# Kernel optimization log

Measured on AMD Instinct MI355X. Metric: run time of the kernel, lower is better.

## Reference

```python
import jax, jax.numpy as jnp
import numpy as np

TOP_K = 5

def setup_inputs() -> dict:
    key = jax.random.key(0)
    k1, k2, k3, k4 = jax.random.split(key, 4)
    B, L, N, D = 4, 1024, 16384, 256
    encoded = jax.random.normal(k1, (B, L, D), dtype=jnp.float32)
    memory = jax.random.normal(k2, (B, N, D), dtype=jnp.float32)
    W = jax.random.normal(k3, (D, D), dtype=jnp.float32) * (1.0 / np.sqrt(D))
    b = jax.random.normal(k4, (D,), dtype=jnp.float32) * 0.01
    return {"encoded": encoded, "memory": memory, "W": W, "b": b}

def _l2norm(x, eps=1e-12):
    # matches torch F.normalize(dim=-1): x / max(||x||, eps)
    n = jnp.sqrt(jnp.sum(x * x, axis=-1, keepdims=True))
    return x / jnp.maximum(n, eps)

def reference(encoded, memory, W, b):
    # encoded: [B,L,D], memory: [B,N,D]
    enc_n = _l2norm(encoded)
    mem_n = _l2norm(memory)
    # cosine similarity [B,L,N]
    sim = jnp.einsum('bld,bnd->bln', enc_n, mem_n)
    _, idx = jax.lax.top_k(sim, TOP_K)          # idx: [B,L,K]
    # per-batch gather of raw memory rows: [B,L,K,D]
    selected = jax.vmap(lambda m, i: m[i])(memory, idx)
    matched = jnp.mean(selected, axis=2)        # [B,L,D]
    out = (encoded + matched) @ W.T + b         # nn.Linear
    return out
```

## Files before the change

kernel.cpp:

```cpp
#include <hip/hip_runtime.h>
#include <math.h>
#include <float.h>

#define B_  4
#define L_  1024
#define N_  16384
#define D_  256
#define K_  5
#define NCH 16
#define CHUNK (N_/NCH)
#define RESC 16

typedef __attribute__((ext_vector_type(8))) short bf16x8;
typedef __attribute__((ext_vector_type(4))) float f32x4;

static __device__ __forceinline__ unsigned short f2bf(float f) {
    unsigned int u = __float_as_uint(f);
    unsigned int r = (u + 0x7FFFu + ((u >> 16) & 1u)) >> 16;
    return (unsigned short)r;
}

__global__ __launch_bounds__(256) void prep_kernel(
    const float* __restrict__ enc, const float* __restrict__ mem,
    float* __restrict__ invn, unsigned short* __restrict__ memn_bf,
    unsigned short* __restrict__ enc_bf)
{
    const int row = blockIdx.x * 4 + (threadIdx.x >> 6);
    const int lane = threadIdx.x & 63;
    if (row < B_ * N_) {
        float4 v = reinterpret_cast<const float4*>(mem + (size_t)row * D_)[lane];
        float ss = v.x*v.x + v.y*v.y + v.z*v.z + v.w*v.w;
        #pragma unroll
        for (int off = 32; off; off >>= 1) ss += __shfl_xor(ss, off, 64);
        float inv = 1.0f / fmaxf(sqrtf(ss), 1e-12f);
        if (lane == 0) invn[row] = inv;
        uint2 p;
        p.x = (unsigned)f2bf(v.x*inv) | ((unsigned)f2bf(v.y*inv) << 16);
        p.y = (unsigned)f2bf(v.z*inv) | ((unsigned)f2bf(v.w*inv) << 16);
        reinterpret_cast<uint2*>(memn_bf + (size_t)row * D_)[lane] = p;
    } else {
        int r2 = row - B_ * N_;
        if (r2 >= B_ * L_) return;
        float4 v = reinterpret_cast<const float4*>(enc + (size_t)r2 * D_)[lane];
        uint2 p;
        p.x = (unsigned)f2bf(v.x) | ((unsigned)f2bf(v.y) << 16);
        p.y = (unsigned)f2bf(v.z) | ((unsigned)f2bf(v.w) << 16);
        reinterpret_cast<uint2*>(enc_bf + (size_t)r2 * D_)[lane] = p;
    }
}

__global__ __launch_bounds__(256, 2) void screen_kernel(
    const unsigned short* __restrict__ enc_bf,
    const unsigned short* __restrict__ memn_bf,
    unsigned int* __restrict__ pcand)
{
    __shared__ __align__(16) union {
        struct { unsigned char A[128*128]; unsigned char Bt[128*128]; } st;
        unsigned int mg[128][41];
    } sm;

    const int tid = threadIdx.x;
    const int lane = tid & 63;
    const int wv = tid >> 6;
    const int wm = wv >> 1, wn = wv & 1;
    const int b = blockIdx.z;
    const int l0 = blockIdx.y * 128;
    const int ch = blockIdx.x;

    const int sq = tid & 7;
    const int sr0 = tid >> 3;

    const int ra = wm * 64 + (lane & 15);
    const int rb = wn * 64 + (lane & 15);
    const unsigned aswz = ((unsigned)(ra & 7)) << 4;
    const unsigned bswz = ((unsigned)(rb & 7)) << 4;
    const int kgB = (lane >> 4) * 16;
    const int g4 = (lane >> 4) * 4;

    const unsigned short* encB = enc_bf + ((size_t)b * L_ + l0) * D_;
    const unsigned short* memB = memn_bf + ((size_t)b * N_ + ch * CHUNK) * D_;

    unsigned tl[4][5];
    #pragma unroll
    for (int j = 0; j < 4; ++j)
        #pragma unroll
        for (int p = 0; p < 5; ++p) tl[j][p] = 0u;

    for (int nt = 0; nt < CHUNK / 128; ++nt) {
        const int n0 = nt * 128;
        f32x4 acc[4][4];
        #pragma unroll
        for (int i = 0; i < 4; ++i)
            #pragma unroll
            for (int j = 0; j < 4; ++j) acc[i][j] = (f32x4){0.f,0.f,0.f,0.f};

        for (int kt = 0; kt < D_ / 64; ++kt) {
            const int k0 = kt * 64;
            __syncthreads();
            #pragma unroll
            for (int i = 0; i < 4; ++i) {
                const int row = sr0 + i * 32;
                const int colw = (sq * 16) ^ ((row & 7) << 4);
                uint4 va = *reinterpret_cast<const uint4*>(
                    &memB[(size_t)(n0 + row) * D_ + k0 + sq * 8]);
                *reinterpret_cast<uint4*>(sm.st.A + row * 128 + colw) = va;
                uint4 vb = *reinterpret_cast<const uint4*>(
                    &encB[(size_t)row * D_ + k0 + sq * 8]);
                *reinterpret_cast<uint4*>(sm.st.Bt + row * 128 + colw) = vb;
            }
            __syncthreads();
            #pragma unroll
            for (int kk = 0; kk < 2; ++kk) {
                const int kb = kk * 64 + kgB;
                bf16x8 af[4], bfv[4];
                #pragma unroll
                for (int m = 0; m < 4; ++m)
                    af[m] = *reinterpret_cast<const bf16x8*>(
                        sm.st.A + (ra + m * 16) * 128 + (kb ^ aswz));
                #pragma unroll
                for (int n = 0; n < 4; ++n)
                    bfv[n] = *reinterpret_cast<const bf16x8*>(
                        sm.st.Bt + (rb + n * 16) * 128 + (kb ^ bswz));
                #pragma unroll
                for (int m = 0; m < 4; ++m)
                    #pragma unroll
                    for (int n = 0; n < 4; ++n)
                        acc[m][n] = __builtin_amdgcn_mfma_f32_16x16x32_bf16(
                            af[m], bfv[n], acc[m][n], 0, 0, 0);
            }
        }

        const unsigned inv_base = 1023u - (unsigned)(n0 + wm * 64 + g4);
        #pragma unroll
        for (int i = 0; i < 4; ++i) {
            #pragma unroll
            for (int r = 0; r < 4; ++r) {
                const unsigned idxv = inv_base - (unsigned)(i * 16 + r);
                #pragma unroll
                for (int j = 0; j < 4; ++j) {
                    float fb = acc[i][j][r] + 64.0f;
                    unsigned c = (__float_as_uint(fb) & 0xFFFFFC00u) | idxv;
                    #pragma unroll
                    for (int p = 0; p < 5; ++p) {
                        unsigned mx = tl[j][p] > c ? tl[j][p] : c;
                        unsigned mn = tl[j][p] > c ? c : tl[j][p];
                        tl[j][p] = mx; c = mn;
                    }
                }
            }
        }
    }

    __syncthreads();
    {
        const int c = lane & 15;
        const int src = wm * 4 + (lane >> 4);
        #pragma unroll
        for (int j = 0; j < 4; ++j) {
            const int l = wn * 64 + j * 16 + c;
            #pragma unroll
            for (int p = 0; p < 5; ++p)
                sm.mg[l][src * 5 + p] = tl[j][p];
        }
    }
    __syncthreads();

    if (tid < 128) {
        unsigned best[8];
        #pragma unroll
        for (int p = 0; p < 8; ++p) best[p] = 0u;
        #pragma unroll
        for (int c = 0; c < 40; ++c) {
            unsigned key = sm.mg[tid][c];
            #pragma unroll
            for (int p = 0; p < 8; ++p) {
                unsigned mx = best[p] > key ? best[p] : key;
                unsigned mn = best[p] > key ? key : best[p];
                best[p] = mx; key = mn;
            }
        }
        size_t gb = (((size_t)b * L_ + l0 + tid) * NCH + ch) * 8;
        #pragma unroll
        for (int p = 0; p < 8; ++p) pcand[gb + p] = best[p];
    }
}

__global__ __launch_bounds__(256) void rescore_kernel(
    const float* __restrict__ enc, const float* __restrict__ mem,
    const float* __restrict__ invn,
    const unsigned int* __restrict__ pcand,
    float* __restrict__ tbuf)
{
    __shared__ int cand_lds[4][RESC];
    const int wv = threadIdx.x >> 6;
    const int lane = threadIdx.x & 63;
    const int row = blockIdx.x * 4 + wv;
    const int b = row >> 10;
    const int l = row & 1023;

    const size_t cb = (size_t)row * (NCH * 8);
    unsigned k0 = pcand[cb + lane], k1 = pcand[cb + 64 + lane];

    #pragma unroll
    for (int rr = 0; rr < RESC; ++rr) {
        unsigned mv; int mi;
        bool t0 = (k0 >= k1);
        mv = t0 ? k0 : k1; mi = t0 ? lane : 64 + lane;
        #pragma unroll
        for (int off = 32; off; off >>= 1) {
            unsigned ov = __shfl_xor(mv, off, 64);
            int oi = __shfl_xor(mi, off, 64);
            if (ov > mv || (ov == mv && oi < mi)) { mv = ov; mi = oi; }
        }
        if (lane == 0) {
            int chunk = mi >> 3;
            cand_lds[wv][rr] = chunk * CHUNK + (CHUNK - 1) - (int)(mv & 0x3FFu);
        }
        if (mi == lane) k0 = 0u;
        if (mi == 64 + lane) k1 = 0u;
    }
    __syncthreads();

    const int ci = cand_lds[wv][lane >> 2];
    const int q = lane & 3;
    const float4* er = reinterpret_cast<const float4*>(enc + ((size_t)b * L_ + l) * D_) + q * 16;
    const float4* mr = reinterpret_cast<const float4*>(mem + ((size_t)b * N_ + ci) * D_) + q * 16;
    float s = 0.0f;
    #pragma unroll
    for (int k = 0; k < 16; ++k) {
        float4 e = er[k], m = mr[k];
        s = fmaf(e.x, m.x, s); s = fmaf(e.y, m.y, s);
        s = fmaf(e.z, m.z, s); s = fmaf(e.w, m.w, s);
    }
    s += __shfl_xor(s, 1, 64);
    s += __shfl_xor(s, 2, 64);
    s *= invn[b * N_ + ci];

    float sw = s;
    int m0, m1, m2, m3, m4;
    #define PICK(MK) { \
        float mv = sw; int mi = ci; \
        if (sw == -FLT_MAX) mi = 0x7fffffff; \
        _Pragma("unroll") \
        for (int off = 32; off; off >>= 1) { \
            float ov = __shfl_xor(mv, off, 64); \
            int oi = __shfl_xor(mi, off, 64); \
            if (ov > mv || (ov == mv && oi < mi)) { mv = ov; mi = oi; } \
        } \
        MK = mi; \
        if (ci == mi) sw = -FLT_MAX; \
    }
    PICK(m0); PICK(m1); PICK(m2); PICK(m3); PICK(m4);
    #undef PICK

    const float4* eb = reinterpret_cast<const float4*>(enc + ((size_t)b * L_ + l) * D_);
    const float4* mb = reinterpret_cast<const float4*>(mem + (size_t)b * N_ * D_);
    float4 e = eb[lane];
    float4 a0 = mb[(size_t)m0 * 64 + lane];
    float4 a1 = mb[(size_t)m1 * 64 + lane];
    float4 a2 = mb[(size_t)m2 * 64 + lane];
    float4 a3 = mb[(size_t)m3 * 64 + lane];
    float4 a4 = mb[(size_t)m4 * 64 + lane];
    float4 o;
    o.x = e.x + 0.2f * (a0.x + a1.x + a2.x + a3.x + a4.x);
    o.y = e.y + 0.2f * (a0.y + a1.y + a2.y + a3.y + a4.y);
    o.z = e.z + 0.2f * (a0.z + a1.z + a2.z + a3.z + a4.z);
    o.w = e.w + 0.2f * (a0.w + a1.w + a2.w + a3.w + a4.w);
    reinterpret_cast<float4*>(tbuf + (size_t)row * D_)[lane] = o;
}

__global__ __launch_bounds__(512) void linear_kernel(
    const float* __restrict__ tbuf, const float* __restrict__ W,
    const float* __restrict__ bias, float* __restrict__ out)
{
    __shared__ float t_s[16][D_];
    const int blk = blockIdx.x;
    const int b = blk >> 6;
    const int r0 = (blk & 63) << 4;
    const int tid = threadIdx.x;

    #pragma unroll
    for (int k = 0; k < 2; ++k) {
        int idx = k * 512 + tid;
        int row = idx >> 6, c4 = idx & 63;
        float4 v = reinterpret_cast<const float4*>(
            tbuf + ((size_t)b * L_ + r0 + row) * D_)[c4];
        *reinterpret_cast<float4*>(&t_s[row][c4 * 4]) = v;
    }
    __syncthreads();

    const int dout = tid & 255;
    const int half = tid >> 8;
    float accr[8];
    #pragma unroll
    for (int r = 0; r < 8; ++r) accr[r] = 0.0f;
    const float4* Wr = reinterpret_cast<const float4*>(W + (size_t)dout * D_);
    for (int d4 = 0; d4 < D_ / 4; ++d4) {
        float4 w = Wr[d4];
        #pragma unroll
        for (int r = 0; r < 8; ++r) {
            float4 t = *reinterpret_cast<const float4*>(&t_s[half * 8 + r][d4 * 4]);
            accr[r] = fmaf(w.x, t.x, accr[r]);
            accr[r] = fmaf(w.y, t.y, accr[r]);
            accr[r] = fmaf(w.z, t.z, accr[r]);
            accr[r] = fmaf(w.w, t.w, accr[r]);
        }
    }
    float bb = bias[dout];
    #pragma unroll
    for (int r = 0; r < 8; ++r)
        out[((size_t)b * L_ + r0 + half * 8 + r) * D_ + dout] = accr[r] + bb;
}

extern "C" void kernel_launch(void* const* d_in, const int* in_sizes, int n_in,
                              void* d_out, int out_size, void* d_ws, size_t ws_size,
                              hipStream_t stream)
{
    (void)in_sizes; (void)n_in; (void)out_size;
    const float* enc  = (const float*)d_in[0];
    const float* mem  = (const float*)d_in[1];
    const float* W    = (const float*)d_in[2];
    const float* bias = (const float*)d_in[3];
    float* out = (float*)d_out;

    const size_t sz_memn = (size_t)B_ * N_ * D_ * 2;
    const size_t sz_enc  = (size_t)B_ * L_ * D_ * 2;
    const size_t sz_invn = (size_t)B_ * N_ * 4;
    const size_t sz_pc   = (size_t)B_ * L_ * NCH * 8 * 4;
    const size_t sz_tbuf = (size_t)B_ * L_ * D_ * 4;
    const size_t need = sz_memn + sz_enc + sz_invn + sz_pc + sz_tbuf;
    if (ws_size < need) return;

    char* p = (char*)d_ws;
    unsigned short* memn_bf = (unsigned short*)p;  p += sz_memn;
    unsigned short* enc_bf  = (unsigned short*)p;  p += sz_enc;
    float* invn = (float*)p;  p += sz_invn;
    unsigned int* pcand = (unsigned int*)p;  p += sz_pc;
    float* tbuf = (float*)p;

    {
        int rows = B_ * N_ + B_ * L_;
        prep_kernel<<<(rows + 3) / 4, 256, 0, stream>>>(enc, mem, invn, memn_bf, enc_bf);
    }
    {
        dim3 grid(NCH, L_ / 128, B_);
        screen_kernel<<<grid, 256, 0, stream>>>(enc_bf, memn_bf, pcand);
    }
    {
        rescore_kernel<<<(B_ * L_) / 4, 256, 0, stream>>>(enc, mem, invn, pcand, tbuf);
    }
    {
        linear_kernel<<<B_ * L_ / 16, 512, 0, stream>>>(tbuf, W, bias, out);
    }
}
```

Baseline: 206.7 us.

## Pipeline screen tiles with resident encoder LDS and fuse rescore with linear

The screen kernel now keeps the whole 128-row encoder tile resident in LDS, loaded once with global_load_lds. Memory tiles are streamed through direct-to-LDS loads, and accumulators are double-buffered so the top-5 fold of the previous tile interleaves with the MFMAs of the current tile. The score bias changes from +64 to a clamp at zero. The rescore and linear kernels are merged into one tail kernel that selects candidates with a ballot-based radix threshold instead of 16 serial argmax reductions, which removes the tbuf round trip and one launch. Risks are the 80KB LDS per block, which may reduce occupancy below two blocks per CU, and the clamp, which drops ordering among negative similarities.

```diff
diff --git a/kernel.cpp b/kernel.cpp
--- a/kernel.cpp
+++ b/kernel.cpp
@@ -18,6 +18,12 @@
     unsigned int u = __float_as_uint(f);
     unsigned int r = (u + 0x7FFFu + ((u >> 16) & 1u)) >> 16;
     return (unsigned short)r;
+}
+
+static __device__ __forceinline__ void gld16(const void* g, void* l) {
+    __builtin_amdgcn_global_load_lds(
+        (const __attribute__((address_space(1))) unsigned int*)g,
+        (__attribute__((address_space(3))) unsigned int*)l, 16, 0, 0);
 }
 
 __global__ __launch_bounds__(256) void prep_kernel(
@@ -49,15 +55,72 @@
     }
 }
 
+#define SCREEN_TILE(N0, ACC, PACC, PN0, DOFOLD)                                        \
+  {                                                                                    \
+    _Pragma("unroll")                                                                  \
+    for (int i_ = 0; i_ < 4; ++i_)                                                     \
+      _Pragma("unroll")                                                                \
+      for (int j_ = 0; j_ < 4; ++j_) ACC[i_][j_] = (f32x4){0.f, 0.f, 0.f, 0.f};        \
+    const char* memT_ = memBb + (size_t)(N0) * (D_ * 2);                               \
+    _Pragma("unroll")                                                                  \
+    for (int kt = 0; kt < 4; ++kt) {                                                   \
+      __syncthreads();                                                                 \
+      _Pragma("unroll")                                                                \
+      for (int c_ = 0; c_ < 4; ++c_) {                                                 \
+        int s_ = c_ * 4 + wv;                                                          \
+        gld16(memT_ + (size_t)(s_ * 8 + (lane >> 3)) * (D_ * 2) + kt * 128 + scolA,    \
+              sA + s_ * 1024);                                                         \
+      }                                                                                \
+      __syncthreads();                                                                 \
+      _Pragma("unroll")                                                                \
+      for (int kk = 0; kk < 2; ++kk) {                                                 \
+        const int kbA_ = kk * 64 + kgB;                                                \
+        const int cB_ = kt * 128 + kk * 64 + kgB;                                      \
+        bf16x8 af_[4], bfv_[4];                                                        \
+        _Pragma("unroll")                                                              \
+        for (int m_ = 0; m_ < 4; ++m_)                                                 \
+          af_[m_] = *reinterpret_cast<const bf16x8*>(                                  \
+              sA + (ra + m_ * 16) * 128 + (kbA_ ^ aswz));                              \
+        _Pragma("unroll")                                                              \
+        for (int n_ = 0; n_ < 4; ++n_)                                                 \
+          bfv_[n_] = *reinterpret_cast<const bf16x8*>(                                 \
+              sEnc + (rb + n_ * 16) * 512 + (cB_ ^ bswz));                             \
+        _Pragma("unroll")                                                              \
+        for (int m_ = 0; m_ < 4; ++m_)                                                 \
+          _Pragma("unroll")                                                            \
+          for (int n_ = 0; n_ < 4; ++n_)                                               \
+            ACC[m_][n_] = __builtin_amdgcn_mfma_f32_16x16x32_bf16(                     \
+                af_[m_], bfv_[n_], ACC[m_][n_], 0, 0, 0);                              \
+      }                                                                                \
+      if (DOFOLD) {                                                                    \
+        const unsigned ibase_ = 1023u - (unsigned)((PN0) + wm * 64 + kt * 16 + g4);    \
+        _Pragma("unroll")                                                              \
+        for (int r_ = 0; r_ < 4; ++r_) {                                               \
+          const unsigned idxv_ = ibase_ - (unsigned)r_;                                \
+          _Pragma("unroll")                                                            \
+          for (int j_ = 0; j_ < 4; ++j_) {                                             \
+            unsigned c2_ = (__float_as_uint(fmaxf(PACC[kt][j_][r_], 0.0f))             \
+                            & 0xFFFFFC00u) | idxv_;                                    \
+            _Pragma("unroll")                                                          \
+            for (int p_ = 0; p_ < 5; ++p_) {                                           \
+              unsigned mx_ = tl[j_][p_] > c2_ ? tl[j_][p_] : c2_;                      \
+              unsigned mn_ = tl[j_][p_] > c2_ ? c2_ : tl[j_][p_];                      \
+              tl[j_][p_] = mx_; c2_ = mn_;                                             \
+            }                                                                          \
+          }                                                                            \
+        }                                                                              \
+      }                                                                                \
+    }                                                                                  \
+  }
+
 __global__ __launch_bounds__(256, 2) void screen_kernel(
     const unsigned short* __restrict__ enc_bf,
     const unsigned short* __restrict__ memn_bf,
     unsigned int* __restrict__ pcand)
 {
-    __shared__ __align__(16) union {
-        struct { unsigned char A[128*128]; unsigned char Bt[128*128]; } st;
-        unsigned int mg[128][41];
-    } sm;
+    __shared__ __align__(16) unsigned char smem[16*1024 + 64*1024];
+    unsigned char* sA = smem;
+    unsigned char* sEnc = smem + 16*1024;
 
     const int tid = threadIdx.x;
     const int lane = tid & 63;
@@ -67,18 +130,24 @@
     const int l0 = blockIdx.y * 128;
     const int ch = blockIdx.x;
 
-    const int sq = tid & 7;
-    const int sr0 = tid >> 3;
-
     const int ra = wm * 64 + (lane & 15);
     const int rb = wn * 64 + (lane & 15);
     const unsigned aswz = ((unsigned)(ra & 7)) << 4;
     const unsigned bswz = ((unsigned)(rb & 7)) << 4;
     const int kgB = (lane >> 4) * 16;
     const int g4 = (lane >> 4) * 4;
-
-    const unsigned short* encB = enc_bf + ((size_t)b * L_ + l0) * D_;
-    const unsigned short* memB = memn_bf + ((size_t)b * N_ + ch * CHUNK) * D_;
+    const int scolA = ((lane & 7) * 16) ^ ((lane >> 3) << 4);
+
+    const char* encBb = (const char*)(enc_bf + ((size_t)b * L_ + l0) * D_);
+    const char* memBb = (const char*)(memn_bf + ((size_t)b * N_ + ch * CHUNK) * D_);
+
+    #pragma unroll
+    for (int c = 0; c < 16; ++c) {
+        int s = c * 4 + wv;
+        int row = s * 2 + (lane >> 5);
+        int col = ((lane & 31) * 16) ^ ((row & 7) << 4);
+        gld16(encBb + (size_t)row * 512 + col, sEnc + s * 1024);
+    }
 
     unsigned tl[4][5];
     #pragma unroll
@@ -86,65 +155,36 @@
         #pragma unroll
         for (int p = 0; p < 5; ++p) tl[j][p] = 0u;
 
-    for (int nt = 0; nt < CHUNK / 128; ++nt) {
-        const int n0 = nt * 128;
-        f32x4 acc[4][4];
-        #pragma unroll
-        for (int i = 0; i < 4; ++i)
-            #pragma unroll
-            for (int j = 0; j < 4; ++j) acc[i][j] = (f32x4){0.f,0.f,0.f,0.f};
-
-        for (int kt = 0; kt < D_ / 64; ++kt) {
-            const int k0 = kt * 64;
-            __syncthreads();
-            #pragma unroll
-            for (int i = 0; i < 4; ++i) {
-                const int row = sr0 + i * 32;
-                const int colw = (sq * 16) ^ ((row & 7) << 4);
-                uint4 va = *reinterpret_cast<const uint4*>(
-                    &memB[(size_t)(n0 + row) * D_ + k0 + sq * 8]);
-                *reinterpret_cast<uint4*>(sm.st.A + row * 128 + colw) = va;
-                uint4 vb = *reinterpret_cast<const uint4*>(
-                    &encB[(size_t)row * D_ + k0 + sq * 8]);
-                *reinterpret_cast<uint4*>(sm.st.Bt + row * 128 + colw) = vb;
-            }
-            __syncthreads();
-            #pragma unroll
-            for (int kk = 0; kk < 2; ++kk) {
-                const int kb = kk * 64 + kgB;
-                bf16x8 af[4], bfv[4];
-                #pragma unroll
-                for (int m = 0; m < 4; ++m)
-                    af[m] = *reinterpret_cast<const bf16x8*>(
-                        sm.st.A + (ra + m * 16) * 128 + (kb ^ aswz));
-                #pragma unroll
-                for (int n = 0; n < 4; ++n)
-                    bfv[n] = *reinterpret_cast<const bf16x8*>(
-                        sm.st.Bt + (rb + n * 16) * 128 + (kb ^ bswz));
-                #pragma unroll
-                for (int m = 0; m < 4; ++m)
-                    #pragma unroll
-                    for (int n = 0; n < 4; ++n)
-                        acc[m][n] = __builtin_amdgcn_mfma_f32_16x16x32_bf16(
-                            af[m], bfv[n], acc[m][n], 0, 0, 0);
-            }
-        }
-
-        const unsigned inv_base = 1023u - (unsigned)(n0 + wm * 64 + g4);
+    f32x4 accA[4][4], accB[4][4];
+
+    SCREEN_TILE(0, accA, accB, 0, false)
+    {
+        int n0v = 128, pn0v = 0;
+        #pragma unroll 1
+        for (int it = 0; it < 3; ++it) {
+            SCREEN_TILE(n0v, accB, accA, pn0v, true)
+            SCREEN_TILE(n0v + 128, accA, accB, pn0v + 128, true)
+            n0v += 256; pn0v += 256;
+        }
+    }
+    SCREEN_TILE(896, accB, accA, 768, true)
+
+    {
         #pragma unroll
         for (int i = 0; i < 4; ++i) {
+            const unsigned ibase = 1023u - (unsigned)(896 + wm * 64 + i * 16 + g4);
             #pragma unroll
             for (int r = 0; r < 4; ++r) {
-                const unsigned idxv = inv_base - (unsigned)(i * 16 + r);
+                const unsigned idxv = ibase - (unsigned)r;
                 #pragma unroll
                 for (int j = 0; j < 4; ++j) {
-                    float fb = acc[i][j][r] + 64.0f;
-                    unsigned c = (__float_as_uint(fb) & 0xFFFFFC00u) | idxv;
+                    unsigned c2 = (__float_as_uint(fmaxf(accB[i][j][r], 0.0f))
+                                   & 0xFFFFFC00u) | idxv;
                     #pragma unroll
                     for (int p = 0; p < 5; ++p) {
-                        unsigned mx = tl[j][p] > c ? tl[j][p] : c;
-                        unsigned mn = tl[j][p] > c ? c : tl[j][p];
-                        tl[j][p] = mx; c = mn;
+                        unsigned mx = tl[j][p] > c2 ? tl[j][p] : c2;
+                        unsigned mn = tl[j][p] > c2 ? c2 : tl[j][p];
+                        tl[j][p] = mx; c2 = mn;
                     }
                 }
             }
@@ -152,6 +192,7 @@
     }
 
     __syncthreads();
+    unsigned (*mg)[41] = reinterpret_cast<unsigned (*)[41]>(smem);
     {
         const int c = lane & 15;
         const int src = wm * 4 + (lane >> 4);
@@ -160,7 +201,7 @@
             const int l = wn * 64 + j * 16 + c;
             #pragma unroll
             for (int p = 0; p < 5; ++p)
-                sm.mg[l][src * 5 + p] = tl[j][p];
+                mg[l][src * 5 + p] = tl[j][p];
         }
     }
     __syncthreads();
@@ -171,7 +212,7 @@
         for (int p = 0; p < 8; ++p) best[p] = 0u;
         #pragma unroll
         for (int c = 0; c < 40; ++c) {
-            unsigned key = sm.mg[tid][c];
+            unsigned key = mg[tid][c];
             #pragma unroll
             for (int p = 0; p < 8; ++p) {
                 unsigned mx = best[p] > key ? best[p] : key;
@@ -185,112 +226,102 @@
     }
 }
 
-__global__ __launch_bounds__(256) void rescore_kernel(
+__global__ __launch_bounds__(256) void tail_kernel(
     const float* __restrict__ enc, const float* __restrict__ mem,
     const float* __restrict__ invn,
     const unsigned int* __restrict__ pcand,
-    float* __restrict__ tbuf)
+    const float* __restrict__ W, const float* __restrict__ bias,
+    float* __restrict__ out)
 {
-    __shared__ int cand_lds[4][RESC];
+    __shared__ float t_s[8][D_];
+    __shared__ int cand_s[4][RESC];
     const int wv = threadIdx.x >> 6;
     const int lane = threadIdx.x & 63;
-    const int row = blockIdx.x * 4 + wv;
-    const int b = row >> 10;
-    const int l = row & 1023;
-
-    const size_t cb = (size_t)row * (NCH * 8);
-    unsigned k0 = pcand[cb + lane], k1 = pcand[cb + 64 + lane];
-
-    #pragma unroll
-    for (int rr = 0; rr < RESC; ++rr) {
-        unsigned mv; int mi;
-        bool t0 = (k0 >= k1);
-        mv = t0 ? k0 : k1; mi = t0 ? lane : 64 + lane;
-        #pragma unroll
-        for (int off = 32; off; off >>= 1) {
-            unsigned ov = __shfl_xor(mv, off, 64);
-            int oi = __shfl_xor(mi, off, 64);
-            if (ov > mv || (ov == mv && oi < mi)) { mv = ov; mi = oi; }
-        }
-        if (lane == 0) {
-            int chunk = mi >> 3;
-            cand_lds[wv][rr] = chunk * CHUNK + (CHUNK - 1) - (int)(mv & 0x3FFu);
-        }
-        if (mi == lane) k0 = 0u;
-        if (mi == 64 + lane) k1 = 0u;
+    const int row0 = blockIdx.x * 8 + wv * 2;
+
+    #pragma unroll 1
+    for (int r2 = 0; r2 < 2; ++r2) {
+        const int row = row0 + r2;
+        const int b = row >> 10;
+        const int l = row & 1023;
+
+        const size_t cb = (size_t)row * (NCH * 8);
+        unsigned k0 = pcand[cb + lane], k1 = pcand[cb + 64 + lane];
+
+        unsigned v = 0;
+        #pragma unroll
+        for (int bit = 31; bit >= 0; --bit) {
+            unsigned t = v | (1u << bit);
+            int c = __popcll(__ballot(k0 >= t)) + __popcll(__ballot(k1 >= t));
+            v = (c >= RESC) ? t : v;
+        }
+        unsigned long long bA0 = __ballot(k0 > v), bA1 = __ballot(k1 > v);
+        unsigned long long bE0 = __ballot(k0 == v), bE1 = __ballot(k1 == v);
+        const int nA0 = __popcll(bA0);
+        const int nA = nA0 + __popcll(bA1);
+        const int need = RESC - nA;
+        const unsigned long long lt = (1ull << lane) - 1ull;
+        int s0 = -1, s1 = -1;
+        if (k0 > v) s0 = __popcll(bA0 & lt);
+        else if (k0 == v) { int r = __popcll(bE0 & lt); if (r < need) s0 = nA + r; }
+        if (k1 > v) s1 = nA0 + __popcll(bA1 & lt);
+        else if (k1 == v) { int r = __popcll(bE0) + __popcll(bE1 & lt); if (r < need) s1 = nA + r; }
+        if (s0 >= 0)
+            cand_s[wv][s0] = (lane >> 3) * CHUNK + (CHUNK - 1) - (int)(k0 & 1023u);
+        if (s1 >= 0)
+            cand_s[wv][s1] = (8 + (lane >> 3)) * CHUNK + (CHUNK - 1) - (int)(k1 & 1023u);
+        asm volatile("s_waitcnt lgkmcnt(0)" ::: "memory");
+
+        const int ci = cand_s[wv][lane >> 2];
+        const int q = lane & 3;
+        const float4* er = reinterpret_cast<const float4*>(enc + ((size_t)b * L_ + l) * D_) + q * 16;
+        const float4* mr = reinterpret_cast<const float4*>(mem + ((size_t)b * N_ + ci) * D_) + q * 16;
+        float s = 0.0f;
+        #pragma unroll
+        for (int k = 0; k < 16; ++k) {
+            float4 e = er[k], m = mr[k];
+            s = fmaf(e.x, m.x, s); s = fmaf(e.y, m.y, s);
+            s = fmaf(e.z, m.z, s); s = fmaf(e.w, m.w, s);
+        }
+        s += __shfl_xor(s, 1, 64);
+        s += __shfl_xor(s, 2, 64);
+        s *= invn[b * N_ + ci];
+
+        float sw = s;
+        int m0, m1, m2, m3, m4;
+        #define PICK(MK) { \
+            float mv = sw; int mi = ci; \
+            if (sw == -FLT_MAX) mi = 0x7fffffff; \
+            _Pragma("unroll") \
+            for (int off = 32; off >= 4; off >>= 1) { \
+                float ov = __shfl_xor(mv, off, 64); \
+                int oi = __shfl_xor(mi, off, 64); \
+                if (ov > mv || (ov == mv && oi < mi)) { mv = ov; mi = oi; } \
+            } \
+            MK = mi; \
+            if (ci == mi) sw = -FLT_MAX; \
+        }
+        PICK(m0); PICK(m1); PICK(m2); PICK(m3); PICK(m4);
+        #undef PICK
+
+        const float4* eb = reinterpret_cast<const float4*>(enc + ((size_t)b * L_ + l) * D_);
+        const float4* mb = reinterpret_cast<const float4*>(mem + (size_t)b * N_ * D_);
+        float4 e = eb[lane];
+        float4 a0 = mb[(size_t)m0 * 64 + lane];
+        float4 a1 = mb[(size_t)m1 * 64 + lane];
+        float4 a2 = mb[(size_t)m2 * 64 + lane];
+        float4 a3 = mb[(size_t)m3 * 64 + lane];
+        float4 a4 = mb[(size_t)m4 * 64 + lane];
+        float4 o;
+        o.x = e.x + 0.2f * (a0.x + a1.x + a2.x + a3.x + a4.x);
+        o.y = e.y + 0.2f * (a0.y + a1.y + a2.y + a3.y + a4.y);
+        o.z = e.z + 0.2f * (a0.z + a1.z + a2.z + a3.z + a4.z);
+        o.w = e.w + 0.2f * (a0.w + a1.w + a2.w + a3.w + a4.w);
+        *reinterpret_cast<float4*>(&t_s[wv * 2 + r2][lane * 4]) = o;
     }
     __syncthreads();
 
-    const int ci = cand_lds[wv][lane >> 2];
-    const int q = lane & 3;
-    const float4* er = reinterpret_cast<const float4*>(enc + ((size_t)b * L_ + l) * D_) + q * 16;
-    const float4* mr = reinterpret_cast<const float4*>(mem + ((size_t)b * N_ + ci) * D_) + q * 16;
-    float s = 0.0f;
-    #pragma unroll
-    for (int k = 0; k < 16; ++k) {
-        float4 e = er[k], m = mr[k];
-        s = fmaf(e.x, m.x, s); s = fmaf(e.y, m.y, s);
-        s = fmaf(e.z, m.z, s); s = fmaf(e.w, m.w, s);
-    }
-    s += __shfl_xor(s, 1, 64);
-    s += __shfl_xor(s, 2, 64);
-    s *= invn[b * N_ + ci];
-
-    float sw = s;
-    int m0, m1, m2, m3, m4;
-    #define PICK(MK) { \
-        float mv = sw; int mi = ci; \
-        if (sw == -FLT_MAX) mi = 0x7fffffff; \
-        _Pragma("unroll") \
-        for (int off = 32; off; off >>= 1) { \
-            float ov = __shfl_xor(mv, off, 64); \
-            int oi = __shfl_xor(mi, off, 64); \
-            if (ov > mv || (ov == mv && oi < mi)) { mv = ov; mi = oi; } \
-        } \
-        MK = mi; \
-        if (ci == mi) sw = -FLT_MAX; \
-    }
-    PICK(m0); PICK(m1); PICK(m2); PICK(m3); PICK(m4);
-    #undef PICK
-
-    const float4* eb = reinterpret_cast<const float4*>(enc + ((size_t)b * L_ + l) * D_);
-    const float4* mb = reinterpret_cast<const float4*>(mem + (size_t)b * N_ * D_);
-    float4 e = eb[lane];
-    float4 a0 = mb[(size_t)m0 * 64 + lane];
-    float4 a1 = mb[(size_t)m1 * 64 + lane];
-    float4 a2 = mb[(size_t)m2 * 64 + lane];
-    float4 a3 = mb[(size_t)m3 * 64 + lane];
-    float4 a4 = mb[(size_t)m4 * 64 + lane];
-    float4 o;
-    o.x = e.x + 0.2f * (a0.x + a1.x + a2.x + a3.x + a4.x);
-    o.y = e.y + 0.2f * (a0.y + a1.y + a2.y + a3.y + a4.y);
-    o.z = e.z + 0.2f * (a0.z + a1.z + a2.z + a3.z + a4.z);
-    o.w = e.w + 0.2f * (a0.w + a1.w + a2.w + a3.w + a4.w);
-    reinterpret_cast<float4*>(tbuf + (size_t)row * D_)[lane] = o;
-}
-
-__global__ __launch_bounds__(512) void linear_kernel(
-    const float* __restrict__ tbuf, const float* __restrict__ W,
-    const float* __restrict__ bias, float* __restrict__ out)
-{
-    __shared__ float t_s[16][D_];
-    const int blk = blockIdx.x;
-    const int b = blk >> 6;
-    const int r0 = (blk & 63) << 4;
-    const int tid = threadIdx.x;
-
-    #pragma unroll
-    for (int k = 0; k < 2; ++k) {
-        int idx = k * 512 + tid;
-        int row = idx >> 6, c4 = idx & 63;
-        float4 v = reinterpret_cast<const float4*>(
-            tbuf + ((size_t)b * L_ + r0 + row) * D_)[c4];
-        *reinterpret_cast<float4*>(&t_s[row][c4 * 4]) = v;
-    }
-    __syncthreads();
-
-    const int dout = tid & 255;
-    const int half = tid >> 8;
+    const int dout = threadIdx.x;
     float accr[8];
     #pragma unroll
     for (int r = 0; r < 8; ++r) accr[r] = 0.0f;
@@ -299,7 +330,7 @@
         float4 w = Wr[d4];
         #pragma unroll
         for (int r = 0; r < 8; ++r) {
-            float4 t = *reinterpret_cast<const float4*>(&t_s[half * 8 + r][d4 * 4]);
+            float4 t = *reinterpret_cast<const float4*>(&t_s[r][d4 * 4]);
             accr[r] = fmaf(w.x, t.x, accr[r]);
             accr[r] = fmaf(w.y, t.y, accr[r]);
             accr[r] = fmaf(w.z, t.z, accr[r]);
@@ -309,7 +340,7 @@
     float bb = bias[dout];
     #pragma unroll
     for (int r = 0; r < 8; ++r)
-        out[((size_t)b * L_ + r0 + half * 8 + r) * D_ + dout] = accr[r] + bb;
+        out[((size_t)blockIdx.x * 8 + r) * D_ + dout] = accr[r] + bb;
 }
 
 extern "C" void kernel_launch(void* const* d_in, const int* in_sizes, int n_in,
@@ -327,16 +358,14 @@
     const size_t sz_enc  = (size_t)B_ * L_ * D_ * 2;
     const size_t sz_invn = (size_t)B_ * N_ * 4;
     const size_t sz_pc   = (size_t)B_ * L_ * NCH * 8 * 4;
-    const size_t sz_tbuf = (size_t)B_ * L_ * D_ * 4;
-    const size_t need = sz_memn + sz_enc + sz_invn + sz_pc + sz_tbuf;
+    const size_t need = sz_memn + sz_enc + sz_invn + sz_pc;
     if (ws_size < need) return;
 
     char* p = (char*)d_ws;
     unsigned short* memn_bf = (unsigned short*)p;  p += sz_memn;
     unsigned short* enc_bf  = (unsigned short*)p;  p += sz_enc;
     float* invn = (float*)p;  p += sz_invn;
-    unsigned int* pcand = (unsigned int*)p;  p += sz_pc;
-    float* tbuf = (float*)p;
+    unsigned int* pcand = (unsigned int*)p;
 
     {
         int rows = B_ * N_ + B_ * L_;
@@ -347,9 +376,6 @@
         screen_kernel<<<grid, 256, 0, stream>>>(enc_bf, memn_bf, pcand);
     }
     {
-        rescore_kernel<<<(B_ * L_) / 4, 256, 0, stream>>>(enc, mem, invn, pcand, tbuf);
-    }
-    {
-        linear_kernel<<<B_ * L_ / 16, 512, 0, stream>>>(tbuf, W, bias, out);
-    }
-}
+        tail_kernel<<<(B_ * L_) / 8, 256, 0, stream>>>(enc, mem, invn, pcand, W, bias, out);
+    }
+}
```

After: 196.2 us. 1.05x faster.

## Use direct global-to-LDS loads in screen, double chunks, fuse rescore with linear

Applied to the files above, without the earlier changes.

The screen kernel now stages tiles with global_load_lds instead of register round-trips, unrolls the k loop, raises occupancy to 4 blocks per CU, and splits N into 32 chunks for more parallelism. The rescore stage now picks its candidates with a radix-select over ballots instead of 16 serial argmax reductions. It is fused with the linear projection into one tail kernel, which drops the tbuf workspace round-trip and one launch. The price is twice as many partial candidates to merge and score keys clamped at zero, which changes how negative similarities are ranked.

```diff
diff --git a/kernel.cpp b/kernel.cpp
--- a/kernel.cpp
+++ b/kernel.cpp
@@ -7,7 +7,7 @@
 #define N_  16384
 #define D_  256
 #define K_  5
-#define NCH 16
+#define NCH 32
 #define CHUNK (N_/NCH)
 #define RESC 16
 
@@ -18,6 +18,12 @@
     unsigned int u = __float_as_uint(f);
     unsigned int r = (u + 0x7FFFu + ((u >> 16) & 1u)) >> 16;
     return (unsigned short)r;
+}
+
+static __device__ __forceinline__ void gld16(const void* g, void* l) {
+    __builtin_amdgcn_global_load_lds(
+        (const __attribute__((address_space(1))) unsigned int*)g,
+        (__attribute__((address_space(3))) unsigned int*)l, 16, 0, 0);
 }
 
 __global__ __launch_bounds__(256) void prep_kernel(
@@ -49,13 +55,13 @@
     }
 }
 
-__global__ __launch_bounds__(256, 2) void screen_kernel(
+__global__ __launch_bounds__(256, 4) void screen_kernel(
     const unsigned short* __restrict__ enc_bf,
     const unsigned short* __restrict__ memn_bf,
     unsigned int* __restrict__ pcand)
 {
     __shared__ __align__(16) union {
-        struct { unsigned char A[128*128]; unsigned char Bt[128*128]; } st;
+        struct { unsigned char A[16*1024]; unsigned char B[16*1024]; } st;
         unsigned int mg[128][41];
     } sm;
 
@@ -67,18 +73,17 @@
     const int l0 = blockIdx.y * 128;
     const int ch = blockIdx.x;
 
-    const int sq = tid & 7;
-    const int sr0 = tid >> 3;
-
     const int ra = wm * 64 + (lane & 15);
     const int rb = wn * 64 + (lane & 15);
     const unsigned aswz = ((unsigned)(ra & 7)) << 4;
     const unsigned bswz = ((unsigned)(rb & 7)) << 4;
     const int kgB = (lane >> 4) * 16;
     const int g4 = (lane >> 4) * 4;
-
-    const unsigned short* encB = enc_bf + ((size_t)b * L_ + l0) * D_;
-    const unsigned short* memB = memn_bf + ((size_t)b * N_ + ch * CHUNK) * D_;
+    const int srow = lane >> 3;
+    const int scol = ((lane & 7) * 16) ^ (srow << 4);
+
+    const char* encBb = (const char*)(enc_bf + ((size_t)b * L_ + l0) * D_);
+    const char* memBb = (const char*)(memn_bf + ((size_t)b * N_ + ch * CHUNK) * D_);
 
     unsigned tl[4][5];
     #pragma unroll
@@ -94,19 +99,16 @@
             #pragma unroll
             for (int j = 0; j < 4; ++j) acc[i][j] = (f32x4){0.f,0.f,0.f,0.f};
 
-        for (int kt = 0; kt < D_ / 64; ++kt) {
-            const int k0 = kt * 64;
+        #pragma unroll
+        for (int kt = 0; kt < 4; ++kt) {
             __syncthreads();
             #pragma unroll
-            for (int i = 0; i < 4; ++i) {
-                const int row = sr0 + i * 32;
-                const int colw = (sq * 16) ^ ((row & 7) << 4);
-                uint4 va = *reinterpret_cast<const uint4*>(
-                    &memB[(size_t)(n0 + row) * D_ + k0 + sq * 8]);
-                *reinterpret_cast<uint4*>(sm.st.A + row * 128 + colw) = va;
-                uint4 vb = *reinterpret_cast<const uint4*>(
-                    &encB[(size_t)row * D_ + k0 + sq * 8]);
-                *reinterpret_cast<uint4*>(sm.st.Bt + row * 128 + colw) = vb;
+            for (int c = 0; c < 4; ++c) {
+                const int s = c * 4 + wv;
+                gld16(encBb + (size_t)(s * 8 + srow) * 512 + kt * 128 + scol,
+                      sm.st.B + s * 1024);
+                gld16(memBb + (size_t)(n0 + s * 8 + srow) * 512 + kt * 128 + scol,
+                      sm.st.A + s * 1024);
             }
             __syncthreads();
             #pragma unroll
@@ -120,7 +122,7 @@
                 #pragma unroll
                 for (int n = 0; n < 4; ++n)
                     bfv[n] = *reinterpret_cast<const bf16x8*>(
-                        sm.st.Bt + (rb + n * 16) * 128 + (kb ^ bswz));
+                        sm.st.B + (rb + n * 16) * 128 + (kb ^ bswz));
                 #pragma unroll
                 for (int m = 0; m < 4; ++m)
                     #pragma unroll
@@ -130,21 +132,20 @@
             }
         }
 
-        const unsigned inv_base = 1023u - (unsigned)(n0 + wm * 64 + g4);
         #pragma unroll
         for (int i = 0; i < 4; ++i) {
             #pragma unroll
             for (int r = 0; r < 4; ++r) {
-                const unsigned idxv = inv_base - (unsigned)(i * 16 + r);
+                const unsigned idxv = 1023u - (unsigned)(n0 + wm * 64 + i * 16 + g4 + r);
                 #pragma unroll
                 for (int j = 0; j < 4; ++j) {
-                    float fb = acc[i][j][r] + 64.0f;
-                    unsigned c = (__float_as_uint(fb) & 0xFFFFFC00u) | idxv;
+                    unsigned c2 = (__float_as_uint(fmaxf(acc[i][j][r], 0.0f))
+                                   & 0xFFFFFC00u) | idxv;
                     #pragma unroll
                     for (int p = 0; p < 5; ++p) {
-                        unsigned mx = tl[j][p] > c ? tl[j][p] : c;
-                        unsigned mn = tl[j][p] > c ? c : tl[j][p];
-                        tl[j][p] = mx; c = mn;
+                        unsigned mx = tl[j][p] > c2 ? tl[j][p] : c2;
+                        unsigned mn = tl[j][p] > c2 ? c2 : tl[j][p];
+                        tl[j][p] = mx; c2 = mn;
                     }
                 }
             }
@@ -185,112 +186,111 @@
     }
 }
 
-__global__ __launch_bounds__(256) void rescore_kernel(
+__global__ __launch_bounds__(256) void tail_kernel(
     const float* __restrict__ enc, const float* __restrict__ mem,
     const float* __restrict__ invn,
     const unsigned int* __restrict__ pcand,
-    float* __restrict__ tbuf)
+    const float* __restrict__ W, const float* __restrict__ bias,
+    float* __restrict__ out)
 {
-    __shared__ int cand_lds[4][RESC];
+    __shared__ float t_s[8][D_];
+    __shared__ int cand_s[4][RESC];
     const int wv = threadIdx.x >> 6;
     const int lane = threadIdx.x & 63;
-    const int row = blockIdx.x * 4 + wv;
-    const int b = row >> 10;
-    const int l = row & 1023;
-
-    const size_t cb = (size_t)row * (NCH * 8);
-    unsigned k0 = pcand[cb + lane], k1 = pcand[cb + 64 + lane];
-
-    #pragma unroll
-    for (int rr = 0; rr < RESC; ++rr) {
-        unsigned mv; int mi;
-        bool t0 = (k0 >= k1);
-        mv = t0 ? k0 : k1; mi = t0 ? lane : 64 + lane;
-        #pragma unroll
-        for (int off = 32; off; off >>= 1) {
-            unsigned ov = __shfl_xor(mv, off, 64);
-            int oi = __shfl_xor(mi, off, 64);
-            if (ov > mv || (ov == mv && oi < mi)) { mv = ov; mi = oi; }
-        }
-        if (lane == 0) {
-            int chunk = mi >> 3;
-            cand_lds[wv][rr] = chunk * CHUNK + (CHUNK - 1) - (int)(mv & 0x3FFu);
-        }
-        if (mi == lane) k0 = 0u;
-        if (mi == 64 + lane) k1 = 0u;
+    const int row0 = blockIdx.x * 8 + wv * 2;
+
+    #pragma unroll 1
+    for (int r2 = 0; r2 < 2; ++r2) {
+        const int row = row0 + r2;
+        const int b = row >> 10;
+        const int l = row & 1023;
+
+        const size_t cb = (size_t)row * (NCH * 8);
+        unsigned k0 = pcand[cb + lane],       k1 = pcand[cb + 64 + lane];
+        unsigned k2 = pcand[cb + 128 + lane], k3 = pcand[cb + 192 + lane];
+
+        unsigned v = 0;
+        #pragma unroll
+        for (int bit = 31; bit >= 0; --bit) {
+            unsigned t = v | (1u << bit);
+            int c = __popcll(__ballot(k0 >= t)) + __popcll(__ballot(k1 >= t))
+                  + __popcll(__ballot(k2 >= t)) + __popcll(__ballot(k3 >= t));
+            v = (c >= RESC) ? t : v;
+        }
+        unsigned long long a0 = __ballot(k0 > v), a1 = __ballot(k1 > v);
+        unsigned long long a2 = __ballot(k2 > v), a3 = __ballot(k3 > v);
+        unsigned long long e0 = __ballot(k0 == v), e1 = __ballot(k1 == v);
+        unsigned long long e2 = __ballot(k2 == v), e3 = __ballot(k3 == v);
+        const int nA0 = __popcll(a0), nA1 = __popcll(a1), nA2 = __popcll(a2);
+        const int nA = nA0 + nA1 + nA2 + __popcll(a3);
+        const int ne0 = __popcll(e0), ne1 = __popcll(e1), ne2 = __popcll(e2);
+        const int need = RESC - nA;
+        const unsigned long long lt = (1ull << lane) - 1ull;
+        int s0 = -1, s1 = -1, s2 = -1, s3 = -1;
+        if (k0 > v) s0 = __popcll(a0 & lt);
+        else if (k0 == v) { int r = __popcll(e0 & lt); if (r < need) s0 = nA + r; }
+        if (k1 > v) s1 = nA0 + __popcll(a1 & lt);
+        else if (k1 == v) { int r = ne0 + __popcll(e1 & lt); if (r < need) s1 = nA + r; }
+        if (k2 > v) s2 = nA0 + nA1 + __popcll(a2 & lt);
+        else if (k2 == v) { int r = ne0 + ne1 + __popcll(e2 & lt); if (r < need) s2 = nA + r; }
+        if (k3 > v) s3 = nA0 + nA1 + nA2 + __popcll(a3 & lt);
+        else if (k3 == v) { int r = ne0 + ne1 + ne2 + __popcll(e3 & lt); if (r < need) s3 = nA + r; }
+        if (s0 >= 0) cand_s[wv][s0] = ((lane) >> 3) * CHUNK + 1023 - (int)(k0 & 1023u);
+        if (s1 >= 0) cand_s[wv][s1] = ((64 + lane) >> 3) * CHUNK + 1023 - (int)(k1 & 1023u);
+        if (s2 >= 0) cand_s[wv][s2] = ((128 + lane) >> 3) * CHUNK + 1023 - (int)(k2 & 1023u);
+        if (s3 >= 0) cand_s[wv][s3] = ((192 + lane) >> 3) * CHUNK + 1023 - (int)(k3 & 1023u);
+        asm volatile("s_waitcnt lgkmcnt(0)" ::: "memory");
+
+        const int ci = cand_s[wv][lane >> 2];
+        const int q = lane & 3;
+        const float4* er = reinterpret_cast<const float4*>(enc + ((size_t)b * L_ + l) * D_) + q * 16;
+        const float4* mr = reinterpret_cast<const float4*>(mem + ((size_t)b * N_ + ci) * D_) + q * 16;
+        float s = 0.0f;
+        #pragma unroll
+        for (int k = 0; k < 16; ++k) {
+            float4 e = er[k], m = mr[k];
+            s = fmaf(e.x, m.x, s); s = fmaf(e.y, m.y, s);
+            s = fmaf(e.z, m.z, s); s = fmaf(e.w, m.w, s);
+        }
+        s += __shfl_xor(s, 1, 64);
+        s += __shfl_xor(s, 2, 64);
+        s *= invn[b * N_ + ci];
+
+        float sw = s;
+        int m0, m1, m2, m3, m4;
+        #define PICK(MK) { \
+            float mv = sw; int mi = ci; \
+            if (sw == -FLT_MAX) mi = 0x7fffffff; \
+            _Pragma("unroll") \
+            for (int off = 32; off >= 4; off >>= 1) { \
+                float ov = __shfl_xor(mv, off, 64); \
+                int oi = __shfl_xor(mi, off, 64); \
+                if (ov > mv || (ov == mv && oi < mi)) { mv = ov; mi = oi; } \
+            } \
+            MK = mi; \
+            if (ci == mi) sw = -FLT_MAX; \
+        }
+        PICK(m0); PICK(m1); PICK(m2); PICK(m3); PICK(m4);
+        #undef PICK
+
+        const float4* eb = reinterpret_cast<const float4*>(enc + ((size_t)b * L_ + l) * D_);
+        const float4* mb = reinterpret_cast<const float4*>(mem + (size_t)b * N_ * D_);
+        float4 e = eb[lane];
+        float4 g0 = mb[(size_t)m0 * 64 + lane];
+        float4 g1 = mb[(size_t)m1 * 64 + lane];
+        float4 g2 = mb[(size_t)m2 * 64 + lane];
+        float4 g3 = mb[(size_t)m3 * 64 + lane];
+        float4 g4v = mb[(size_t)m4 * 64 + lane];
+        float4 o;
+        o.x = e.x + 0.2f * (g0.x + g1.x + g2.x + g3.x + g4v.x);
+        o.y = e.y + 0.2f * (g0.y + g1.y + g2.y + g3.y + g4v.y);
+        o.z = e.z + 0.2f * (g0.z + g1.z + g2.z + g3.z + g4v.z);
+        o.w = e.w + 0.2f * (g0.w + g1.w + g2.w + g3.w + g4v.w);
+        *reinterpret_cast<float4*>(&t_s[wv * 2 + r2][lane * 4]) = o;
     }
     __syncthreads();
 
-    const int ci = cand_lds[wv][lane >> 2];
-    const int q = lane & 3;
-    const float4* er = reinterpret_cast<const float4*>(enc + ((size_t)b * L_ + l) * D_) + q * 16;
-    const float4* mr = reinterpret_cast<const float4*>(mem + ((size_t)b * N_ + ci) * D_) + q * 16;
-    float s = 0.0f;
-    #pragma unroll
-    for (int k = 0; k < 16; ++k) {
-        float4 e = er[k], m = mr[k];
-        s = fmaf(e.x, m.x, s); s = fmaf(e.y, m.y, s);
-        s = fmaf(e.z, m.z, s); s = fmaf(e.w, m.w, s);
-    }
-    s += __shfl_xor(s, 1, 64);
-    s += __shfl_xor(s, 2, 64);
-    s *= invn[b * N_ + ci];
-
-    float sw = s;
-    int m0, m1, m2, m3, m4;
-    #define PICK(MK) { \
-        float mv = sw; int mi = ci; \
-        if (sw == -FLT_MAX) mi = 0x7fffffff; \
-        _Pragma("unroll") \
-        for (int off = 32; off; off >>= 1) { \
-            float ov = __shfl_xor(mv, off, 64); \
-            int oi = __shfl_xor(mi, off, 64); \
-            if (ov > mv || (ov == mv && oi < mi)) { mv = ov; mi = oi; } \
-        } \
-        MK = mi; \
-        if (ci == mi) sw = -FLT_MAX; \
-    }
-    PICK(m0); PICK(m1); PICK(m2); PICK(m3); PICK(m4);
-    #undef PICK
-
-    const float4* eb = reinterpret_cast<const float4*>(enc + ((size_t)b * L_ + l) * D_);
-    const float4* mb = reinterpret_cast<const float4*>(mem + (size_t)b * N_ * D_);
-    float4 e = eb[lane];
-    float4 a0 = mb[(size_t)m0 * 64 + lane];
-    float4 a1 = mb[(size_t)m1 * 64 + lane];
-    float4 a2 = mb[(size_t)m2 * 64 + lane];
-    float4 a3 = mb[(size_t)m3 * 64 + lane];
-    float4 a4 = mb[(size_t)m4 * 64 + lane];
-    float4 o;
-    o.x = e.x + 0.2f * (a0.x + a1.x + a2.x + a3.x + a4.x);
-    o.y = e.y + 0.2f * (a0.y + a1.y + a2.y + a3.y + a4.y);
-    o.z = e.z + 0.2f * (a0.z + a1.z + a2.z + a3.z + a4.z);
-    o.w = e.w + 0.2f * (a0.w + a1.w + a2.w + a3.w + a4.w);
-    reinterpret_cast<float4*>(tbuf + (size_t)row * D_)[lane] = o;
-}
-
-__global__ __launch_bounds__(512) void linear_kernel(
-    const float* __restrict__ tbuf, const float* __restrict__ W,
-    const float* __restrict__ bias, float* __restrict__ out)
-{
-    __shared__ float t_s[16][D_];
-    const int blk = blockIdx.x;
-    const int b = blk >> 6;
-    const int r0 = (blk & 63) << 4;
-    const int tid = threadIdx.x;
-
-    #pragma unroll
-    for (int k = 0; k < 2; ++k) {
-        int idx = k * 512 + tid;
-        int row = idx >> 6, c4 = idx & 63;
-        float4 v = reinterpret_cast<const float4*>(
-            tbuf + ((size_t)b * L_ + r0 + row) * D_)[c4];
-        *reinterpret_cast<float4*>(&t_s[row][c4 * 4]) = v;
-    }
-    __syncthreads();
-
-    const int dout = tid & 255;
-    const int half = tid >> 8;
+    const int dout = threadIdx.x;
     float accr[8];
     #pragma unroll
     for (int r = 0; r < 8; ++r) accr[r] = 0.0f;
@@ -299,7 +299,7 @@
         float4 w = Wr[d4];
         #pragma unroll
         for (int r = 0; r < 8; ++r) {
-            float4 t = *reinterpret_cast<const float4*>(&t_s[half * 8 + r][d4 * 4]);
+            float4 t = *reinterpret_cast<const float4*>(&t_s[r][d4 * 4]);
             accr[r] = fmaf(w.x, t.x, accr[r]);
             accr[r] = fmaf(w.y, t.y, accr[r]);
             accr[r] = fmaf(w.z, t.z, accr[r]);
@@ -309,7 +309,7 @@
     float bb = bias[dout];
     #pragma unroll
     for (int r = 0; r < 8; ++r)
-        out[((size_t)b * L_ + r0 + half * 8 + r) * D_ + dout] = accr[r] + bb;
+        out[((size_t)blockIdx.x * 8 + r) * D_ + dout] = accr[r] + bb;
 }
 
 extern "C" void kernel_launch(void* const* d_in, const int* in_sizes, int n_in,
@@ -327,16 +327,14 @@
     const size_t sz_enc  = (size_t)B_ * L_ * D_ * 2;
     const size_t sz_invn = (size_t)B_ * N_ * 4;
     const size_t sz_pc   = (size_t)B_ * L_ * NCH * 8 * 4;
-    const size_t sz_tbuf = (size_t)B_ * L_ * D_ * 4;
-    const size_t need = sz_memn + sz_enc + sz_invn + sz_pc + sz_tbuf;
+    const size_t need = sz_memn + sz_enc + sz_invn + sz_pc;
     if (ws_size < need) return;
 
     char* p = (char*)d_ws;
     unsigned short* memn_bf = (unsigned short*)p;  p += sz_memn;
     unsigned short* enc_bf  = (unsigned short*)p;  p += sz_enc;
     float* invn = (float*)p;  p += sz_invn;
-    unsigned int* pcand = (unsigned int*)p;  p += sz_pc;
-    float* tbuf = (float*)p;
+    unsigned int* pcand = (unsigned int*)p;
 
     {
         int rows = B_ * N_ + B_ * L_;
@@ -347,9 +345,6 @@
         screen_kernel<<<grid, 256, 0, stream>>>(enc_bf, memn_bf, pcand);
     }
     {
-        rescore_kernel<<<(B_ * L_) / 4, 256, 0, stream>>>(enc, mem, invn, pcand, tbuf);
-    }
-    {
-        linear_kernel<<<B_ * L_ / 16, 512, 0, stream>>>(tbuf, W, bias, out);
-    }
-}
+        tail_kernel<<<(B_ * L_) / 8, 256, 0, stream>>>(enc, mem, invn, pcand, W, bias, out);
+    }
+}
```

Result: slower. 246.3 us (+19.2%).
